# Optimization experiments

Measured on AMD Instinct MI355X. Metric: run time of the kernel, lower is better.

## Reference

```python
import jax, jax.numpy as jnp
import numpy as np

N, E, D_IN, D_OUT = 50000, 300000, 256, 256
BN_EPS = 1e-5


def ccorr(a, b):
    # circular correlation: irfft(conj(rfft(a)) * rfft(b))
    return jnp.fft.irfft(jnp.conj(jnp.fft.rfft(a, axis=-1)) * jnp.fft.rfft(b, axis=-1), n=a.shape[-1], axis=-1)


def setup_inputs() -> dict:
    key = jax.random.key(0)
    ks = jax.random.split(key, 8)
    return {
        "node_ft": jax.random.normal(ks[0], (N, D_IN), dtype=jnp.float32),
        "edge_ft": jax.random.normal(ks[1], (E, D_IN), dtype=jnp.float32),
        "norm": jax.random.uniform(ks[2], (N, 1), dtype=jnp.float32),
        "w_loop": jax.random.normal(ks[3], (D_IN, D_OUT), dtype=jnp.float32) * (1.414 / np.sqrt(D_IN)),
        "w_in": jax.random.normal(ks[4], (D_IN, D_OUT), dtype=jnp.float32) * (1.414 / np.sqrt(D_IN)),
        "loop_rel": jax.random.normal(ks[5], (1, D_IN), dtype=jnp.float32),
        "w_bias": jnp.zeros((D_OUT,), dtype=jnp.float32),
        "bn_gamma": jnp.ones((D_OUT,), dtype=jnp.float32),
        "bn_beta": jnp.zeros((D_OUT,), dtype=jnp.float32),
        "src": jax.random.randint(ks[6], (E,), 0, N, dtype=jnp.int32),
        "dst": jax.random.randint(ks[7], (E,), 0, N, dtype=jnp.int32),
    }


def reference(node_ft, edge_ft, norm, w_loop, w_in, loop_rel, w_bias, bn_gamma, bn_beta, src, dst):
    n_nodes = node_ft.shape[0]
    # self-loop message: ccorr(ft, loop_rel) @ w_loop  [N, d_out]
    loop_msg = ccorr(node_ft, loop_rel) @ w_loop
    # per-edge message: ccorr(src_ft, edge_ft) @ w_in  [E, d_out]
    msg = ccorr(node_ft[src], edge_ft) @ w_in
    # scatter-sum aggregation then norm multiply (apply_func)
    agg = jax.ops.segment_sum(msg, dst, num_segments=n_nodes) * norm
    h = agg + w_bias + loop_msg
    # BatchNorm1d (training mode: batch stats, biased variance)
    mean = jnp.mean(h, axis=0)
    var = jnp.var(h, axis=0)
    h = (h - mean) * jax.lax.rsqrt(var + BN_EPS) * bn_gamma + bn_beta
    return jnp.tanh(h)
```

## Files before the change

### kernel.cpp

```cpp
#include <hip/hip_runtime.h>
#include <hip/hip_bf16.h>

#define NN 50000
#define EE 300000
#define BN_EPS 1e-5f
#define NFW 288
#define TWOPI_256 0.024543692606170259f

typedef __attribute__((ext_vector_type(8))) _Float16 half8;
typedef __attribute__((ext_vector_type(2))) _Float16 half2v;
typedef __attribute__((ext_vector_type(4))) float f32x4;
#define MFMA16F __builtin_amdgcn_mfma_f32_16x16x32_f16

__device__ __align__(16) _Float16 g_NF[(size_t)NN * NFW];
__device__ float g_Wle[256 * 256];
__device__ float g_C256[256];
__device__ __align__(16) unsigned short g_FB[8 * 20 * 64 * 8];
__device__ __align__(16) unsigned short g_CB[9 * 16 * 64 * 8];
__device__ __align__(16) unsigned short g_WLEB[8 * 16 * 64 * 8];
__device__ int g_hist[NN];
__device__ int g_off[NN + 1];
__device__ int g_cursor[NN];
__device__ int g_perm[EE];
__device__ int g_bsum[128];
__device__ int g_bbase[128];

__device__ __forceinline__ void atomAddF(float* p, float v) { unsafeAtomicAdd(p, v); }

__device__ __forceinline__ unsigned short f2hu(float x) {
    union { _Float16 f; unsigned short u; } c;
    c.f = (_Float16)x;
    return c.u;
}

__device__ __forceinline__ void stage_write(char* A, const float4* stg, int t) {
#pragma unroll
    for (int q = 0; q < 8; ++q) {
        int idx = q * 512 + t;
        int row = idx >> 6, c4 = idx & 63;
        union { _Float16 f[4]; ushort4 u; } r;
        r.f[0] = (_Float16)stg[q].x; r.f[1] = (_Float16)stg[q].y;
        r.f[2] = (_Float16)stg[q].z; r.f[3] = (_Float16)stg[q].w;
        int ks = c4 >> 3;
        int off = ((row >> 4) * 8 + ks) * 1024 +
                  ((((((c4 >> 1) & 3) << 4) | (row & 15)) * 16) ^ (ks << 4)) +
                  (c4 & 1) * 8;
        *(ushort4*)(A + off) = r.u;
    }
}

__device__ __forceinline__ float waveSum(float v) {
#pragma unroll
    for (int d = 1; d < 64; d <<= 1) v += __shfl_xor(v, d);
    return v;
}

__global__ __launch_bounds__(512) void hist_kernel(const int* __restrict__ dst, int E) {
    int e = blockIdx.x * 512 + threadIdx.x;
    if (e < E) atomicAdd(&g_hist[dst[e]], 1);
}

__global__ __launch_bounds__(512) void scanA_kernel(int N) {
    __shared__ int arr[512];
    int t = threadIdx.x, b = blockIdx.x * 512 + t;
    int cnt = (b < N) ? g_hist[b] : 0;
    arr[t] = cnt;
    __syncthreads();
#pragma unroll
    for (int off = 1; off < 512; off <<= 1) {
        int v = (t >= off) ? arr[t - off] : 0;
        __syncthreads();
        arr[t] += v;
        __syncthreads();
    }
    if (b < N) g_off[b] = arr[t] - cnt;
    if (t == 511) g_bsum[blockIdx.x] = arr[511];
}

__global__ __launch_bounds__(128) void scanB_kernel(int nblk) {
    __shared__ int arr[128];
    int t = threadIdx.x;
    int v0 = (t < nblk) ? g_bsum[t] : 0;
    arr[t] = v0;
    __syncthreads();
#pragma unroll
    for (int off = 1; off < 128; off <<= 1) {
        int v = (t >= off) ? arr[t - off] : 0;
        __syncthreads();
        arr[t] += v;
        __syncthreads();
    }
    if (t < nblk) g_bbase[t] = arr[t] - v0;
}

__global__ __launch_bounds__(512) void scanC_kernel(int N) {
    int b = blockIdx.x * 512 + threadIdx.x;
    if (b < N) {
        int v = g_off[b] + g_bbase[blockIdx.x];
        g_off[b] = v;
        g_cursor[b] = v;
        if (b == N - 1) g_off[N] = v + g_hist[b];
    }
}

__global__ __launch_bounds__(512) void perm_kernel(const int* __restrict__ dst, int E) {
    int e = blockIdx.x * 512 + threadIdx.x;
    if (e < E) {
        int pos = atomicAdd(&g_cursor[dst[e]], 1);
        g_perm[pos] = e;
    }
}

__global__ __launch_bounds__(256) void wle_kernel(
    const float* __restrict__ loop_rel, const float* __restrict__ w_loop,
    float* __restrict__ W_le) {
    __shared__ float lr[256];
    const int d = threadIdx.x, j = blockIdx.x;
    lr[d] = loop_rel[d];
    __syncthreads();
    float acc = 0.f;
#pragma unroll 4
    for (int k = 0; k < 256; ++k)
        acc = fmaf(lr[(j + k) & 255], w_loop[k * 256 + d], acc);
    W_le[j * 256 + d] = acc;
}

__global__ __launch_bounds__(512) void fb_pack() {
    int b = blockIdx.x, ks = b / 20, nt = b % 20;
    int t = threadIdx.x, lane = t >> 3, e = t & 7;
    int k = 32 * ks + 8 * (lane >> 4) + e;
    int r2 = nt * 16 + (lane & 15);
    float val = 0.f;
    if (r2 < 258) {
        int f = r2 >> 1;
        int m = (f * k) & 255;
        float s, c;
        sincosf((float)m * TWOPI_256, &s, &c);
        val = (r2 & 1) ? -s : c;
    }
    g_FB[((ks * 20 + nt) * 64 + lane) * 8 + e] = f2hu(val);
}

__global__ __launch_bounds__(512) void cb_pack(const float* __restrict__ w_in) {
    __shared__ float ct[256], st[256];
    int t = threadIdx.x;
    if (t < 256) {
        float s, c;
        sincosf((float)t * TWOPI_256, &s, &c);
        ct[t] = c; st[t] = s;
    }
    __syncthreads();
    int b = blockIdx.x, ks = b / 16, nt = b % 16;
    int lane = t >> 3, e = t & 7;
    int kk = 32 * ks + 8 * (lane >> 4) + e;
    int d = nt * 16 + (lane & 15);
    float val = 0.f;
    if (kk < 258) {
        int f = kk >> 1;
        float cf = (f == 0 || f == 128) ? (1.f / 256.f) : (2.f / 256.f);
        const float* tab = (kk & 1) ? st : ct;
        float sgn = (kk & 1) ? -1.f : 1.f;
        float acc = 0.f;
        for (int k = 0; k < 256; ++k)
            acc = fmaf(tab[(f * k) & 255], w_in[k * 256 + d], acc);
        val = cf * sgn * acc;
    }
    if (kk == 256) g_C256[d] = val;
    g_CB[((ks * 16 + nt) * 64 + lane) * 8 + e] = f2hu(val);
}

__global__ __launch_bounds__(512) void wleb_pack() {
    int b = blockIdx.x, ks = b / 16, nt = b % 16;
    int t = threadIdx.x, lane = t >> 3, e = t & 7;
    int k = 32 * ks + 8 * (lane >> 4) + e;
    int d = nt * 16 + (lane & 15);
    g_WLEB[((ks * 16 + nt) * 64 + lane) * 8 + e] = f2hu(g_Wle[k * 256 + d]);
}

__global__ __launch_bounds__(512, 4) void nfloop_kernel(
    const float* __restrict__ node_ft, const float* __restrict__ w_bias,
    float* __restrict__ out, int N) {
    __shared__ char smem[32768];
    unsigned short* A = (unsigned short*)smem;
    const int t = threadIdx.x;
    const int wv = t >> 6;
    const long long r0 = (long long)blockIdx.x * 64;
    {
        float4 stg[8];
#pragma unroll
        for (int q = 0; q < 8; ++q) {
            int idx = q * 512 + t;
            long long gr = r0 + (idx >> 6);
            if (gr >= N) gr = N - 1;
            stg[q] = ((const float4*)node_ft)[gr * 64 + (idx & 63)];
        }
#pragma unroll
        for (int q = 0; q < 8; ++q) {
            float c = stg[q].x - stg[q].y + stg[q].z - stg[q].w;
            c = waveSum(c);
            int row = q * 8 + wv;
            if ((t & 63) == 0 && r0 + row < N)
                g_NF[(r0 + row) * NFW + 256] = (_Float16)c;
        }
        stage_write(smem, stg, t);
    }
    __syncthreads();

    const int lane = t & 63;
    const int mw = wv >> 2, nw = wv & 3;
    const int l15 = lane & 15, lg = lane >> 4;

    {
        f32x4 acc[2][4] = {};
#pragma unroll
        for (int ks = 0; ks < 8; ++ks) {
            half8 a0 = *(const half8*)((char*)A + ((2 * mw + 0) * 8 + ks) * 1024 + ((lane * 16) ^ (ks << 4)));
            half8 a1 = *(const half8*)((char*)A + ((2 * mw + 1) * 8 + ks) * 1024 + ((lane * 16) ^ (ks << 4)));
#pragma unroll
            for (int j = 0; j < 4; ++j) {
                int tn = nw + 4 * j;
                half8 bf = *(const half8*)(g_FB + ((size_t)(ks * 20 + tn) * 64 + lane) * 8);
                acc[0][j] = MFMA16F(a0, bf, acc[0][j], 0, 0, 0);
                acc[1][j] = MFMA16F(a1, bf, acc[1][j], 0, 0, 0);
            }
        }
#pragma unroll
        for (int mt = 0; mt < 2; ++mt)
#pragma unroll
            for (int j = 0; j < 4; ++j) {
                int r2 = (nw + 4 * j) * 16 + l15;
#pragma unroll
                for (int r = 0; r < 4; ++r) {
                    long long gr = r0 + (2 * mw + mt) * 16 + lg * 4 + r;
                    if (gr < N) g_NF[gr * NFW + r2] = (_Float16)acc[mt][j][r];
                }
            }
    }
    {
        f32x4 acc[2][4] = {};
#pragma unroll
        for (int ks = 0; ks < 8; ++ks) {
            half8 a0 = *(const half8*)((char*)A + ((2 * mw + 0) * 8 + ks) * 1024 + ((lane * 16) ^ (ks << 4)));
            half8 a1 = *(const half8*)((char*)A + ((2 * mw + 1) * 8 + ks) * 1024 + ((lane * 16) ^ (ks << 4)));
#pragma unroll
            for (int j = 0; j < 4; ++j) {
                half8 bf = *(const half8*)(g_WLEB + ((size_t)(ks * 16 + 4 * nw + j) * 64 + lane) * 8);
                acc[0][j] = MFMA16F(a0, bf, acc[0][j], 0, 0, 0);
                acc[1][j] = MFMA16F(a1, bf, acc[1][j], 0, 0, 0);
            }
        }
#pragma unroll
        for (int j = 0; j < 4; ++j) {
            const int col = (4 * nw + j) * 16 + l15;
            const float bj = w_bias[col];
#pragma unroll
            for (int mt = 0; mt < 2; ++mt)
#pragma unroll
                for (int r = 0; r < 4; ++r) {
                    long long gr = r0 + (2 * mw + mt) * 16 + lg * 4 + r;
                    if (gr < N)
                        out[gr * 256 + col] = acc[mt][j][r] + bj;
                }
        }
    }
}

__global__ __launch_bounds__(512, 6) void edge_kernel(
    const float* __restrict__ edge_ft, const float* __restrict__ norm,
    const int* __restrict__ src, const int* __restrict__ dst,
    float* __restrict__ agg, int E) {
    __shared__ char smem[32768 + 1024];
    unsigned short* A = (unsigned short*)smem;
    unsigned short* Z = (unsigned short*)smem;
    int*   sdd  = (int*)(smem + 32768);
    float* snrm = (float*)(smem + 32768 + 256);
    int*   ssrc = (int*)(smem + 32768 + 512);
    float* nyq  = (float*)(smem + 32768 + 768);

    const int t = threadIdx.x;
    const long long ebase = (long long)blockIdx.x * 64;
    const int lane = t & 63, wv = t >> 6;
    const int mw = wv >> 2, nw = wv & 3;
    const int l15 = lane & 15, lg = lane >> 4;
    const bool odd = (l15 & 1);

    if (t < 64) {
        long long ge = ebase + t;
        if (ge >= E) ge = E - 1;
        int p = g_perm[ge];
        int d = dst[p];
        sdd[t] = d;
        snrm[t] = norm[d];
        ssrc[t] = src[p];
    }

    {
        float4 stg[8];
#pragma unroll
        for (int q = 0; q < 8; ++q) {
            long long ge = ebase + q * 8 + wv;
            if (ge >= E) ge = E - 1;
            stg[q] = ((const float4*)edge_ft)[(long long)g_perm[ge] * 64 + lane];
        }
#pragma unroll
        for (int q = 0; q < 8; ++q) {
            float c = stg[q].x - stg[q].y + stg[q].z - stg[q].w;
            c = waveSum(c);
            if (lane == 0) nyq[q * 8 + wv] = c;
        }
        stage_write(smem, stg, t);
    }
    __syncthreads();

    f32x4 acc1[2][4] = {};
#pragma unroll
    for (int ks = 0; ks < 8; ++ks) {
        half8 a0 = *(const half8*)((char*)A + ((2 * mw + 0) * 8 + ks) * 1024 + ((lane * 16) ^ (ks << 4)));
        half8 a1 = *(const half8*)((char*)A + ((2 * mw + 1) * 8 + ks) * 1024 + ((lane * 16) ^ (ks << 4)));
#pragma unroll
        for (int j = 0; j < 4; ++j) {
            int tn = nw + 4 * j;
            half8 bf = *(const half8*)(g_FB + ((size_t)(ks * 20 + tn) * 64 + lane) * 8);
            acc1[0][j] = MFMA16F(a0, bf, acc1[0][j], 0, 0, 0);
            acc1[1][j] = MFMA16F(a1, bf, acc1[1][j], 0, 0, 0);
        }
    }
    __syncthreads();

    if (t < 64)
        nyq[t] = nyq[t] * (float)g_NF[(size_t)ssrc[t] * NFW + 256];

#pragma unroll
    for (int mt = 0; mt < 2; ++mt) {
        int tm = 2 * mw + mt;
#pragma unroll
        for (int r = 0; r < 4; ++r) {
            int e = tm * 16 + lg * 4 + r;
            const char* nfrow = (const char*)(g_NF + (size_t)ssrc[e] * NFW);
#pragma unroll
            for (int j = 0; j < 4; ++j) {
                int r2 = (nw + 4 * j) * 16 + l15;
                float own = acc1[mt][j][r];
                float oth = __shfl_xor(own, 1);
                union { unsigned int u; half2v h; } cv;
                cv.u = *(const unsigned int*)(nfrow + (r2 & ~1) * 2);
                float br = (float)cv.h[0], bi = (float)cv.h[1];
                float z = odd ? (br * own - bi * oth) : (br * own + bi * oth);
                int ksz = r2 >> 5;
                int off = (tm * 8 + ksz) * 1024 +
                          ((((((r2 >> 3) & 3) << 4) | (e & 15)) * 16) ^ (ksz << 4)) +
                          (r2 & 7) * 2;
                *(unsigned short*)((char*)Z + off) = f2hu(z);
            }
        }
    }
    __syncthreads();

    f32x4 acc2[2][4] = {};
#pragma unroll
    for (int ks = 0; ks < 8; ++ks) {
        half8 a0 = *(const half8*)((char*)Z + ((2 * mw + 0) * 8 + ks) * 1024 + ((lane * 16) ^ (ks << 4)));
        half8 a1 = *(const half8*)((char*)Z + ((2 * mw + 1) * 8 + ks) * 1024 + ((lane * 16) ^ (ks << 4)));
#pragma unroll
        for (int j = 0; j < 4; ++j) {
            half8 bf = *(const half8*)(g_CB + ((size_t)(ks * 16 + 4 * nw + j) * 64 + lane) * 8);
            acc2[0][j] = MFMA16F(a0, bf, acc2[0][j], 0, 0, 0);
            acc2[1][j] = MFMA16F(a1, bf, acc2[1][j], 0, 0, 0);
        }
    }
    {
        float c256[4];
#pragma unroll
        for (int j = 0; j < 4; ++j) c256[j] = g_C256[(4 * nw + j) * 16 + l15];
#pragma unroll
        for (int mt = 0; mt < 2; ++mt)
#pragma unroll
            for (int r = 0; r < 4; ++r) {
                float zn = nyq[(2 * mw + mt) * 16 + lg * 4 + r];
#pragma unroll
                for (int j = 0; j < 4; ++j)
                    acc2[mt][j][r] = fmaf(zn, c256[j], acc2[mt][j][r]);
            }
    }

#pragma unroll
    for (int mt = 0; mt < 2; ++mt) {
        const int e0 = (2 * mw + mt) * 16 + lg * 4;
        const bool v0 = ebase + e0 < E, v1 = ebase + e0 + 1 < E;
        const bool v2 = ebase + e0 + 2 < E, v3 = ebase + e0 + 3 < E;
        const int d0 = sdd[e0], d1 = sdd[e0 + 1], d2 = sdd[e0 + 2], d3 = sdd[e0 + 3];
        const float n0 = snrm[e0], n1 = snrm[e0 + 1], n2 = snrm[e0 + 2], n3 = snrm[e0 + 3];
        const bool uni = v3 && (d0 == d1) && (d1 == d2) && (d2 == d3);
        const bool p01 = v1 && (d0 == d1);
        const bool p23 = v3 && (d2 == d3);
#pragma unroll
        for (int j = 0; j < 4; ++j) {
            const int col = (4 * nw + j) * 16 + l15;
            float x0 = acc2[mt][j][0] * n0, x1 = acc2[mt][j][1] * n1;
            float x2 = acc2[mt][j][2] * n2, x3 = acc2[mt][j][3] * n3;
            if (uni) {
                atomAddF(agg + (long long)d0 * 256 + col, (x0 + x1) + (x2 + x3));
            } else {
                if (p01) atomAddF(agg + (long long)d0 * 256 + col, x0 + x1);
                else {
                    if (v0) atomAddF(agg + (long long)d0 * 256 + col, x0);
                    if (v1) atomAddF(agg + (long long)d1 * 256 + col, x1);
                }
                if (p23) atomAddF(agg + (long long)d2 * 256 + col, x2 + x3);
                else {
                    if (v2) atomAddF(agg + (long long)d2 * 256 + col, x2);
                    if (v3) atomAddF(agg + (long long)d3 * 256 + col, x3);
                }
            }
        }
    }
}

__global__ __launch_bounds__(256) void stats_kernel(
    const float* __restrict__ h, float* __restrict__ s1g,
    float* __restrict__ s2g, long long tot4) {
    __shared__ float s1l[256], s2l[256];
    const int t = threadIdx.x;
    s1l[t] = 0.f;
    s2l[t] = 0.f;
    __syncthreads();
    const int dg = t & 63;
    float a1[4] = {0.f, 0.f, 0.f, 0.f}, a2[4] = {0.f, 0.f, 0.f, 0.f};
    const long long stride = (long long)gridDim.x * 256;
    for (long long i4 = (long long)blockIdx.x * 256 + t; i4 < tot4; i4 += stride) {
        float4 v = ((const float4*)h)[i4];
        a1[0] += v.x; a2[0] += v.x * v.x;
        a1[1] += v.y; a2[1] += v.y * v.y;
        a1[2] += v.z; a2[2] += v.z * v.z;
        a1[3] += v.w; a2[3] += v.w * v.w;
    }
#pragma unroll
    for (int c = 0; c < 4; ++c) {
        atomicAdd(&s1l[dg * 4 + c], a1[c]);
        atomicAdd(&s2l[dg * 4 + c], a2[c]);
    }
    __syncthreads();
    atomAddF(&s1g[t], s1l[t]);
    atomAddF(&s2g[t], s2l[t]);
}

__global__ __launch_bounds__(256) void finalize_kernel(
    float* __restrict__ out, const float* __restrict__ s1g,
    const float* __restrict__ s2g, const float* __restrict__ gamma,
    const float* __restrict__ beta, int N) {
    long long i4 = (long long)blockIdx.x * blockDim.x + threadIdx.x;
    long long tot = (long long)N * 64;
    if (i4 >= tot) return;
    const int dg = (int)(i4 & 63);
    float4 h = ((float4*)out)[i4];
    const float4 s1 = ((const float4*)s1g)[dg];
    const float4 s2 = ((const float4*)s2g)[dg];
    const float4 g = ((const float4*)gamma)[dg];
    const float4 b = ((const float4*)beta)[dg];
    const float invN = 1.f / (float)N;
    float4 o;
    { float m = s1.x * invN; float v = s2.x * invN - m * m;
      o.x = tanhf(fmaf(h.x - m, rsqrtf(v + BN_EPS) * g.x, b.x)); }
    { float m = s1.y * invN; float v = s2.y * invN - m * m;
      o.y = tanhf(fmaf(h.y - m, rsqrtf(v + BN_EPS) * g.y, b.y)); }
    { float m = s1.z * invN; float v = s2.z * invN - m * m;
      o.z = tanhf(fmaf(h.z - m, rsqrtf(v + BN_EPS) * g.z, b.z)); }
    { float m = s1.w * invN; float v = s2.w * invN - m * m;
      o.w = tanhf(fmaf(h.w - m, rsqrtf(v + BN_EPS) * g.w, b.w)); }
    ((float4*)out)[i4] = o;
}

extern "C" void kernel_launch(void* const* d_in, const int* in_sizes, int n_in,
                              void* d_out, int out_size, void* d_ws, size_t ws_size,
                              hipStream_t stream) {
    const float* node_ft  = (const float*)d_in[0];
    const float* edge_ft  = (const float*)d_in[1];
    const float* norm     = (const float*)d_in[2];
    const float* w_loop   = (const float*)d_in[3];
    const float* w_in     = (const float*)d_in[4];
    const float* loop_rel = (const float*)d_in[5];
    const float* w_bias   = (const float*)d_in[6];
    const float* bn_gamma = (const float*)d_in[7];
    const float* bn_beta  = (const float*)d_in[8];
    const int*   src      = (const int*)d_in[9];
    const int*   dst      = (const int*)d_in[10];

    const int N = in_sizes[2];
    const int E = in_sizes[9];
    float* out = (float*)d_out;

    float* s1g = (float*)d_ws;
    float* s2g = s1g + 256;

    hipMemsetAsync(d_ws, 0, 512 * sizeof(float), stream);

    float* Wle_ptr = nullptr;
    hipGetSymbolAddress((void**)&Wle_ptr, HIP_SYMBOL(g_Wle));
    void* hist_ptr = nullptr;
    hipGetSymbolAddress(&hist_ptr, HIP_SYMBOL(g_hist));
    hipMemsetAsync(hist_ptr, 0, (size_t)N * sizeof(int), stream);

    const int sblk = (N + 511) / 512;
    const int eblk = (E + 511) / 512;

    hist_kernel<<<eblk, 512, 0, stream>>>(dst, E);
    scanA_kernel<<<sblk, 512, 0, stream>>>(N);
    scanB_kernel<<<1, 128, 0, stream>>>(sblk);
    scanC_kernel<<<sblk, 512, 0, stream>>>(N);
    perm_kernel<<<eblk, 512, 0, stream>>>(dst, E);

    wle_kernel<<<256, 256, 0, stream>>>(loop_rel, w_loop, Wle_ptr);
    fb_pack<<<8 * 20, 512, 0, stream>>>();
    cb_pack<<<9 * 16, 512, 0, stream>>>(w_in);
    wleb_pack<<<8 * 16, 512, 0, stream>>>();

    nfloop_kernel<<<(N + 63) / 64, 512, 0, stream>>>(node_ft, w_bias, out, N);
    edge_kernel<<<(E + 63) / 64, 512, 0, stream>>>(edge_ft, norm, src, dst, out, E);
    stats_kernel<<<256, 256, 0, stream>>>(out, s1g, s2g, (long long)N * 64);
    finalize_kernel<<<(int)(((long long)N * 64 + 255) / 256), 256, 0, stream>>>(
        out, s1g, s2g, bn_gamma, bn_beta, N);
}
```

Before: 455.7 us.

## Remap edge tiles per XCD, relax edge launch bounds, widen stats grid

Block indices in the edge kernel are remapped so each of the 8 XCDs handles a contiguous range of dst-sorted edge tiles. This is meant to keep scatter-add atomics to the same destination rows within one XCD's L2. The edge kernel's launch-bounds occupancy hint drops from 6 to 4, giving the compiler more registers per thread at the cost of fewer resident waves. The stats kernel grid goes from 256 to 1024 blocks for more parallelism in the reduction.

```diff
diff --git a/kernel.cpp b/kernel.cpp
--- a/kernel.cpp
+++ b/kernel.cpp
@@ -6,6 +6,7 @@
 #define BN_EPS 1e-5f
 #define NFW 288
 #define TWOPI_256 0.024543692606170259f
+#define NXCD 8
 
 typedef __attribute__((ext_vector_type(8))) _Float16 half8;
 typedef __attribute__((ext_vector_type(2))) _Float16 half2v;
@@ -265,7 +266,7 @@
     }
 }
 
-__global__ __launch_bounds__(512, 6) void edge_kernel(
+__global__ __launch_bounds__(512, 4) void edge_kernel(
     const float* __restrict__ edge_ft, const float* __restrict__ norm,
     const int* __restrict__ src, const int* __restrict__ dst,
     float* __restrict__ agg, int E) {
@@ -277,8 +278,13 @@
     int*   ssrc = (int*)(smem + 32768 + 512);
     float* nyq  = (float*)(smem + 32768 + 768);
 
+    const int nwg = gridDim.x;
+    const int q = nwg >> 3, r = nwg & 7;
+    const int xcd = blockIdx.x & 7, idx = blockIdx.x >> 3;
+    const int tile = (xcd < r ? xcd * (q + 1) : r * (q + 1) + (xcd - r) * q) + idx;
+
     const int t = threadIdx.x;
-    const long long ebase = (long long)blockIdx.x * 64;
+    const long long ebase = (long long)tile * 64;
     const int lane = t & 63, wv = t >> 6;
     const int mw = wv >> 2, nw = wv & 3;
     const int l15 = lane & 15, lg = lane >> 4;
@@ -297,16 +303,16 @@
     {
         float4 stg[8];
 #pragma unroll
-        for (int q = 0; q < 8; ++q) {
-            long long ge = ebase + q * 8 + wv;
+        for (int q2 = 0; q2 < 8; ++q2) {
+            long long ge = ebase + q2 * 8 + wv;
             if (ge >= E) ge = E - 1;
-            stg[q] = ((const float4*)edge_ft)[(long long)g_perm[ge] * 64 + lane];
-        }
-#pragma unroll
-        for (int q = 0; q < 8; ++q) {
-            float c = stg[q].x - stg[q].y + stg[q].z - stg[q].w;
+            stg[q2] = ((const float4*)edge_ft)[(long long)g_perm[ge] * 64 + lane];
+        }
+#pragma unroll
+        for (int q2 = 0; q2 < 8; ++q2) {
+            float c = stg[q2].x - stg[q2].y + stg[q2].z - stg[q2].w;
             c = waveSum(c);
-            if (lane == 0) nyq[q * 8 + wv] = c;
+            if (lane == 0) nyq[q2 * 8 + wv] = c;
         }
         stage_write(smem, stg, t);
     }
@@ -334,13 +340,13 @@
     for (int mt = 0; mt < 2; ++mt) {
         int tm = 2 * mw + mt;
 #pragma unroll
-        for (int r = 0; r < 4; ++r) {
-            int e = tm * 16 + lg * 4 + r;
+        for (int r2i = 0; r2i < 4; ++r2i) {
+            int e = tm * 16 + lg * 4 + r2i;
             const char* nfrow = (const char*)(g_NF + (size_t)ssrc[e] * NFW);
 #pragma unroll
             for (int j = 0; j < 4; ++j) {
                 int r2 = (nw + 4 * j) * 16 + l15;
-                float own = acc1[mt][j][r];
+                float own = acc1[mt][j][r2i];
                 float oth = __shfl_xor(own, 1);
                 union { unsigned int u; half2v h; } cv;
                 cv.u = *(const unsigned int*)(nfrow + (r2 & ~1) * 2);
@@ -375,11 +381,11 @@
 #pragma unroll
         for (int mt = 0; mt < 2; ++mt)
 #pragma unroll
-            for (int r = 0; r < 4; ++r) {
-                float zn = nyq[(2 * mw + mt) * 16 + lg * 4 + r];
+            for (int r2i = 0; r2i < 4; ++r2i) {
+                float zn = nyq[(2 * mw + mt) * 16 + lg * 4 + r2i];
 #pragma unroll
                 for (int j = 0; j < 4; ++j)
-                    acc2[mt][j][r] = fmaf(zn, c256[j], acc2[mt][j][r]);
+                    acc2[mt][j][r2i] = fmaf(zn, c256[j], acc2[mt][j][r2i]);
             }
     }
 
@@ -516,7 +522,7 @@
 
     nfloop_kernel<<<(N + 63) / 64, 512, 0, stream>>>(node_ft, w_bias, out, N);
     edge_kernel<<<(E + 63) / 64, 512, 0, stream>>>(edge_ft, norm, src, dst, out, E);
-    stats_kernel<<<256, 256, 0, stream>>>(out, s1g, s2g, (long long)N * 64);
+    stats_kernel<<<1024, 256, 0, stream>>>(out, s1g, s2g, (long long)N * 64);
     finalize_kernel<<<(int)(((long long)N * 64 + 255) / 256), 256, 0, stream>>>(
         out, s1g, s2g, bn_gamma, bn_beta, N);
 }
```

Measured after the change: 430.4 us. 1.06x faster.
